# Optimization experiments

Hardware: AMD Instinct MI355X
Metric: run time of the kernel (lower is better)

The kernel has to match this reference:

```python
import jax, jax.numpy as jnp
import numpy as np

D_MODEL = 4096
N_EXPERTS = 64
TOKENS = 16384


def setup_inputs() -> dict:
    key = jax.random.key(0)
    kx, kw = jax.random.split(key)
    x = jax.random.normal(kx, (TOKENS, D_MODEL), dtype=jnp.float32)
    # nn.Linear(d_model, n_experts, bias=False) weight: [E, d_model]
    wg = jax.random.normal(kw, (N_EXPERTS, D_MODEL), dtype=jnp.float32) * (1.0 / np.sqrt(D_MODEL))
    return {"x": x, "wg": wg, "k": 2}


def reference(x, wg, k):
    S = x.shape[0]
    E = wg.shape[0]
    logits = jnp.einsum('sd,ed->se', x, wg)        # [S, E]
    probs = jax.nn.softmax(logits, axis=-1)        # [S, E]
    topk_vals, topk_idx = jax.lax.top_k(probs, k)  # [S, k] each
    importance = probs.mean(axis=0)                # [E]
    hard1 = topk_idx[:, 0]                         # [S]
    load = jax.ops.segment_sum(jnp.ones((S,), probs.dtype), hard1,
                               num_segments=E) / S  # [E]
    aux_load = E * (importance * load).sum()
    return (topk_idx, topk_vals, aux_load)
```

## Files before the change

kernel.cpp:

```cpp
#include <hip/hip_runtime.h>
#include <cmath>

#define TOKENS 16384
#define DM     4096
#define NEXP   64
#define S_W    64.0f
#define S_LO   2048.0f

typedef _Float16 half8 __attribute__((ext_vector_type(8)));
typedef float    f32x4 __attribute__((ext_vector_type(4)));


__global__ __launch_bounds__(64)
void prep_kernel(const float* __restrict__ wg, _Float16* __restrict__ whB,
                 _Float16* __restrict__ wlB, float* __restrict__ gsum)
{
    const int kb = blockIdx.x >> 2;
    const int et = blockIdx.x & 3;
    const int l  = threadIdx.x;
    const int e  = et * 16 + (l & 15);
    const int k0 = kb * 32 + 8 * (l >> 4);

    const float* wp = wg + (size_t)e * DM + k0;
    float v[8];
    *(float4*)(v)     = *(const float4*)(wp);
    *(float4*)(v + 4) = *(const float4*)(wp + 4);

    half8 hh, ll;
    #pragma unroll
    for (int j = 0; j < 8; ++j) {
        const float ws = v[j] * S_W;
        const _Float16 h = (_Float16)ws;
        hh[j] = h;
        ll[j] = (_Float16)((ws - (float)h) * S_LO);
    }
    const int idx = blockIdx.x * 64 + l;
    ((half8*)whB)[idx] = hh;
    ((half8*)wlB)[idx] = ll;

    if (blockIdx.x == 0) { gsum[l] = 0.f; gsum[64 + l] = 0.f; }
}

__global__ __launch_bounds__(256)
void moe_kernel(const float* __restrict__ x, const _Float16* __restrict__ whB,
                const _Float16* __restrict__ wlB, float* __restrict__ out,
                float* __restrict__ gsum)
{
    const int lane  = threadIdx.x & 63;
    const int wave  = threadIdx.x >> 6;
    const int tgrp  = wave & 1;
    const int khalf = wave >> 1;
    const int sub   = lane & 15;
    const int q     = lane >> 4;
    const int t0    = blockIdx.x * 32 + tgrp * 16;

    f32x4 ahh[4] = {};
    f32x4 amd[4] = {};

    const float* xp = x + (size_t)(t0 + sub) * DM + 8 * q;
    const half8* whv = (const half8*)whB;
    const half8* wlv = (const half8*)wlB;

    const int kb0 = khalf * 64, kbe = kb0 + 64;
    float4 a0 = *(const float4*)(xp + kb0 * 32);
    float4 a1 = *(const float4*)(xp + kb0 * 32 + 4);

    for (int kb = kb0; kb < kbe; ++kb) {
        const int kn = (kb + 1 < kbe) ? kb + 1 : kb;
        float4 n0 = *(const float4*)(xp + kn * 32);
        float4 n1 = *(const float4*)(xp + kn * 32 + 4);

        half8 bh[4], bl[4];
        const int bbase = kb * 256 + lane;
        #pragma unroll
        for (int et = 0; et < 4; ++et) {
            bh[et] = whv[bbase + et * 64];
            bl[et] = wlv[bbase + et * 64];
        }

        float v[8];
        *(float4*)(v)     = a0;
        *(float4*)(v + 4) = a1;
        half8 xh, xl;
        #pragma unroll
        for (int j = 0; j < 8; ++j) {
            const _Float16 h = (_Float16)v[j];
            xh[j] = h;
            xl[j] = (_Float16)((v[j] - (float)h) * S_LO);
        }

        #pragma unroll
        for (int et = 0; et < 4; ++et) {
            ahh[et] = __builtin_amdgcn_mfma_f32_16x16x32_f16(xh, bh[et], ahh[et], 0, 0, 0);
            amd[et] = __builtin_amdgcn_mfma_f32_16x16x32_f16(xh, bl[et], amd[et], 0, 0, 0);
            amd[et] = __builtin_amdgcn_mfma_f32_16x16x32_f16(xl, bh[et], amd[et], 0, 0, 0);
        }
        a0 = n0; a1 = n1;
    }

    float lg[4][4];
    #pragma unroll
    for (int et = 0; et < 4; ++et)
        #pragma unroll
        for (int r = 0; r < 4; ++r)
            lg[et][r] = (ahh[et][r] + amd[et][r] * (1.0f / S_LO)) * (1.0f / S_W);

    __shared__ float lmerge[2][16][64];
    __shared__ float bimp[2][64], bcnt[2][64];

    if (khalf == 1) {
        #pragma unroll
        for (int et = 0; et < 4; ++et)
            #pragma unroll
            for (int r = 0; r < 4; ++r)
                lmerge[tgrp][4 * q + r][sub + 16 * et] = lg[et][r];
    }
    __syncthreads();

    if (khalf == 0) {
        float imp[4] = {0, 0, 0, 0}, cnt[4] = {0, 0, 0, 0};
        #pragma unroll
        for (int et = 0; et < 4; ++et)
            #pragma unroll
            for (int r = 0; r < 4; ++r)
                lg[et][r] += lmerge[tgrp][4 * q + r][sub + 16 * et];

        for (int r = 0; r < 4; ++r) {
            const int tok = t0 + 4 * q + r;
            float m = fmaxf(fmaxf(lg[0][r], lg[1][r]), fmaxf(lg[2][r], lg[3][r]));
            #pragma unroll
            for (int off = 1; off < 16; off <<= 1) m = fmaxf(m, __shfl_xor(m, off));
            float p[4]; float s = 0.f;
            #pragma unroll
            for (int et = 0; et < 4; ++et) { p[et] = expf(lg[et][r] - m); s += p[et]; }
            #pragma unroll
            for (int off = 1; off < 16; off <<= 1) s += __shfl_xor(s, off);
            #pragma unroll
            for (int et = 0; et < 4; ++et) p[et] = p[et] / s;

            float v1, v2; int i1, i2;
            if (p[1] > p[0]) { v1 = p[1]; i1 = sub + 16; v2 = p[0]; i2 = sub; }
            else             { v1 = p[0]; i1 = sub;      v2 = p[1]; i2 = sub + 16; }
            #pragma unroll
            for (int et = 2; et < 4; ++et) {
                const float vv = p[et]; const int id = sub + 16 * et;
                if (vv > v1)      { v2 = v1; i2 = i1; v1 = vv; i1 = id; }
                else if (vv > v2) { v2 = vv; i2 = id; }
            }
            #pragma unroll
            for (int off = 1; off < 16; off <<= 1) {
                const float w1 = __shfl_xor(v1, off), w2 = __shfl_xor(v2, off);
                const int   j1 = __shfl_xor(i1, off), j2 = __shfl_xor(i2, off);
                if (w1 > v1 || (w1 == v1 && j1 < i1)) {
                    if (v1 > w2 || (v1 == w2 && i1 < j2)) { v2 = v1; i2 = i1; }
                    else                                   { v2 = w2; i2 = j2; }
                    v1 = w1; i1 = j1;
                } else {
                    if (w1 > v2 || (w1 == v2 && j1 < i2)) { v2 = w1; i2 = j1; }
                }
            }

            if (sub == 0) {
                out[2 * tok]                  = (float)i1;
                out[2 * tok + 1]              = (float)i2;
                out[2 * TOKENS + 2 * tok]     = v1;
                out[2 * TOKENS + 2 * tok + 1] = v2;
            }
            #pragma unroll
            for (int et = 0; et < 4; ++et) {
                imp[et] += p[et];
                if (i1 == sub + 16 * et) cnt[et] += 1.0f;
            }
        }
        #pragma unroll
        for (int et = 0; et < 4; ++et) {
            imp[et] += __shfl_xor(imp[et], 16); imp[et] += __shfl_xor(imp[et], 32);
            cnt[et] += __shfl_xor(cnt[et], 16); cnt[et] += __shfl_xor(cnt[et], 32);
        }
        if (q == 0) {
            #pragma unroll
            for (int et = 0; et < 4; ++et) {
                bimp[tgrp][sub + 16 * et] = imp[et];
                bcnt[tgrp][sub + 16 * et] = cnt[et];
            }
        }
    }
    __syncthreads();

    if (wave == 0) {
        atomicAdd(gsum + lane,      bimp[0][lane] + bimp[1][lane]);
        atomicAdd(gsum + 64 + lane, bcnt[0][lane] + bcnt[1][lane]);
    }
}

__global__ __launch_bounds__(64)
void aux_kernel(const float* __restrict__ gsum, float* __restrict__ out)
{
    const int l = threadIdx.x;
    float prod = gsum[l] * gsum[64 + l];
    #pragma unroll
    for (int off = 32; off; off >>= 1) prod += __shfl_xor(prod, off);
    if (l == 0)
        out[4 * TOKENS] = (float)NEXP * prod / ((float)TOKENS * (float)TOKENS);
}

extern "C" void kernel_launch(void* const* d_in, const int* in_sizes, int n_in,
                              void* d_out, int out_size, void* d_ws, size_t ws_size,
                              hipStream_t stream) {
    const float* x  = (const float*)d_in[0];
    const float* wg = (const float*)d_in[1];
    float* out = (float*)d_out;

    _Float16* whB = (_Float16*)d_ws;
    _Float16* wlB = whB + 262144;
    float*    gsum = (float*)(wlB + 262144);

    prep_kernel<<<512, 64, 0, stream>>>(wg, whB, wlB, gsum);
    moe_kernel<<<512, 256, 0, stream>>>(x, whB, wlB, out, gsum);
    aux_kernel<<<1, 64, 0, stream>>>(gsum, out);
}
```

Baseline: 405.5 us.

## Deepen x prefetch, double-buffer weights, fuse aux reduction into main kernel

```diff
diff --git a/kernel.cpp b/kernel.cpp
--- a/kernel.cpp
+++ b/kernel.cpp
@@ -7,8 +7,9 @@
 #define S_W    64.0f
 #define S_LO   2048.0f
 
-typedef _Float16 half8 __attribute__((ext_vector_type(8)));
-typedef float    f32x4 __attribute__((ext_vector_type(4)));
+typedef _Float16 half8  __attribute__((ext_vector_type(8)));
+typedef __fp16   h2rtz  __attribute__((ext_vector_type(2)));
+typedef float    f32x4  __attribute__((ext_vector_type(4)));
 
 
 __global__ __launch_bounds__(64)
@@ -23,8 +24,8 @@
 
     const float* wp = wg + (size_t)e * DM + k0;
     float v[8];
-    *(float4*)(v)     = *(const float4*)(wp);
-    *(float4*)(v + 4) = *(const float4*)(wp + 4);
+    *(f32x4*)(v)     = *(const f32x4*)(wp);
+    *(f32x4*)(v + 4) = *(const f32x4*)(wp + 4);
 
     half8 hh, ll;
     #pragma unroll
@@ -38,10 +39,45 @@
     ((half8*)whB)[idx] = hh;
     ((half8*)wlB)[idx] = ll;
 
-    if (blockIdx.x == 0) { gsum[l] = 0.f; gsum[64 + l] = 0.f; }
-}
-
-__global__ __launch_bounds__(256)
+    if (blockIdx.x == 0) {
+        gsum[l] = 0.f; gsum[64 + l] = 0.f;
+        if (l == 0) *(unsigned*)(gsum + 128) = 0u;
+    }
+}
+
+__device__ __forceinline__ void split8(const f32x4& a0, const f32x4& a1,
+                                       half8& xh, half8& xl)
+{
+    float v[8];
+    *(f32x4*)(v)     = a0;
+    *(f32x4*)(v + 4) = a1;
+    h2rtz h01 = __builtin_amdgcn_cvt_pkrtz(v[0], v[1]);
+    h2rtz h23 = __builtin_amdgcn_cvt_pkrtz(v[2], v[3]);
+    h2rtz h45 = __builtin_amdgcn_cvt_pkrtz(v[4], v[5]);
+    h2rtz h67 = __builtin_amdgcn_cvt_pkrtz(v[6], v[7]);
+    xh[0] = (_Float16)h01[0]; xh[1] = (_Float16)h01[1];
+    xh[2] = (_Float16)h23[0]; xh[3] = (_Float16)h23[1];
+    xh[4] = (_Float16)h45[0]; xh[5] = (_Float16)h45[1];
+    xh[6] = (_Float16)h67[0]; xh[7] = (_Float16)h67[1];
+    const float r0 = (v[0] - (float)h01[0]) * S_LO;
+    const float r1 = (v[1] - (float)h01[1]) * S_LO;
+    const float r2 = (v[2] - (float)h23[0]) * S_LO;
+    const float r3 = (v[3] - (float)h23[1]) * S_LO;
+    const float r4 = (v[4] - (float)h45[0]) * S_LO;
+    const float r5 = (v[5] - (float)h45[1]) * S_LO;
+    const float r6 = (v[6] - (float)h67[0]) * S_LO;
+    const float r7 = (v[7] - (float)h67[1]) * S_LO;
+    h2rtz l01 = __builtin_amdgcn_cvt_pkrtz(r0, r1);
+    h2rtz l23 = __builtin_amdgcn_cvt_pkrtz(r2, r3);
+    h2rtz l45 = __builtin_amdgcn_cvt_pkrtz(r4, r5);
+    h2rtz l67 = __builtin_amdgcn_cvt_pkrtz(r6, r7);
+    xl[0] = (_Float16)l01[0]; xl[1] = (_Float16)l01[1];
+    xl[2] = (_Float16)l23[0]; xl[3] = (_Float16)l23[1];
+    xl[4] = (_Float16)l45[0]; xl[5] = (_Float16)l45[1];
+    xl[6] = (_Float16)l67[0]; xl[7] = (_Float16)l67[1];
+}
+
+__global__ __launch_bounds__(256, 2)
 void moe_kernel(const float* __restrict__ x, const _Float16* __restrict__ whB,
                 const _Float16* __restrict__ wlB, float* __restrict__ out,
                 float* __restrict__ gsum)
@@ -62,40 +98,48 @@
     const half8* wlv = (const half8*)wlB;
 
     const int kb0 = khalf * 64, kbe = kb0 + 64;
-    float4 a0 = *(const float4*)(xp + kb0 * 32);
-    float4 a1 = *(const float4*)(xp + kb0 * 32 + 4);
-
-    for (int kb = kb0; kb < kbe; ++kb) {
-        const int kn = (kb + 1 < kbe) ? kb + 1 : kb;
-        float4 n0 = *(const float4*)(xp + kn * 32);
-        float4 n1 = *(const float4*)(xp + kn * 32 + 4);
-
-        half8 bh[4], bl[4];
-        const int bbase = kb * 256 + lane;
-        #pragma unroll
-        for (int et = 0; et < 4; ++et) {
-            bh[et] = whv[bbase + et * 64];
-            bl[et] = wlv[bbase + et * 64];
-        }
-
-        float v[8];
-        *(float4*)(v)     = a0;
-        *(float4*)(v + 4) = a1;
-        half8 xh, xl;
-        #pragma unroll
-        for (int j = 0; j < 8; ++j) {
-            const _Float16 h = (_Float16)v[j];
-            xh[j] = h;
-            xl[j] = (_Float16)((v[j] - (float)h) * S_LO);
-        }
-
-        #pragma unroll
-        for (int et = 0; et < 4; ++et) {
-            ahh[et] = __builtin_amdgcn_mfma_f32_16x16x32_f16(xh, bh[et], ahh[et], 0, 0, 0);
-            amd[et] = __builtin_amdgcn_mfma_f32_16x16x32_f16(xh, bl[et], amd[et], 0, 0, 0);
-            amd[et] = __builtin_amdgcn_mfma_f32_16x16x32_f16(xl, bh[et], amd[et], 0, 0, 0);
-        }
-        a0 = n0; a1 = n1;
+
+    f32x4 ra0[4], ra1[4];
+    #pragma unroll
+    for (int d = 0; d < 3; ++d) {
+        ra0[d] = __builtin_nontemporal_load((const f32x4*)(xp + (kb0 + d) * 32));
+        ra1[d] = __builtin_nontemporal_load((const f32x4*)(xp + (kb0 + d) * 32 + 4));
+    }
+
+    half8 bh[2][4], bl[2][4];
+    #pragma unroll
+    for (int et = 0; et < 4; ++et) {
+        bh[0][et] = whv[kb0 * 256 + lane + et * 64];
+        bl[0][et] = wlv[kb0 * 256 + lane + et * 64];
+    }
+
+    for (int kb = kb0; kb < kbe; kb += 4) {
+        #pragma unroll
+        for (int u = 0; u < 4; ++u) {
+            const int k = kb + u;
+
+            const int kpf = (k + 3 < kbe) ? k + 3 : kbe - 1;
+            ra0[(u + 3) & 3] = __builtin_nontemporal_load((const f32x4*)(xp + kpf * 32));
+            ra1[(u + 3) & 3] = __builtin_nontemporal_load((const f32x4*)(xp + kpf * 32 + 4));
+
+            const int knb = (k + 1 < kbe) ? k + 1 : kbe - 1;
+            const int cur = u & 1, nxt = cur ^ 1;
+            #pragma unroll
+            for (int et = 0; et < 4; ++et) {
+                bh[nxt][et] = whv[knb * 256 + lane + et * 64];
+                bl[nxt][et] = wlv[knb * 256 + lane + et * 64];
+            }
+
+            half8 xh, xl;
+            split8(ra0[u], ra1[u], xh, xl);
+
+            #pragma unroll
+            for (int et = 0; et < 4; ++et) {
+                ahh[et] = __builtin_amdgcn_mfma_f32_16x16x32_f16(xh, bh[cur][et], ahh[et], 0, 0, 0);
+                amd[et] = __builtin_amdgcn_mfma_f32_16x16x32_f16(xh, bl[cur][et], amd[et], 0, 0, 0);
+                amd[et] = __builtin_amdgcn_mfma_f32_16x16x32_f16(xl, bh[cur][et], amd[et], 0, 0, 0);
+            }
+        }
     }
 
     float lg[4][4];
@@ -190,18 +234,24 @@
     if (wave == 0) {
         atomicAdd(gsum + lane,      bimp[0][lane] + bimp[1][lane]);
         atomicAdd(gsum + 64 + lane, bcnt[0][lane] + bcnt[1][lane]);
-    }
-}
-
-__global__ __launch_bounds__(64)
-void aux_kernel(const float* __restrict__ gsum, float* __restrict__ out)
-{
-    const int l = threadIdx.x;
-    float prod = gsum[l] * gsum[64 + l];
-    #pragma unroll
-    for (int off = 32; off; off >>= 1) prod += __shfl_xor(prod, off);
-    if (l == 0)
-        out[4 * TOKENS] = (float)NEXP * prod / ((float)TOKENS * (float)TOKENS);
+        __threadfence();
+        int last = 0;
+        if (lane == 0) {
+            unsigned old = atomicAdd((unsigned*)(gsum + 128), 1u);
+            last = (old == 511u);
+        }
+        last = __shfl(last, 0);
+        if (last) {
+            __threadfence();
+            const float a = atomicAdd(gsum + lane, 0.f);
+            const float b = atomicAdd(gsum + 64 + lane, 0.f);
+            float prod = a * b;
+            #pragma unroll
+            for (int off = 32; off; off >>= 1) prod += __shfl_xor(prod, off);
+            if (lane == 0)
+                out[4 * TOKENS] = (float)NEXP * prod / ((float)TOKENS * (float)TOKENS);
+        }
+    }
 }
 
 extern "C" void kernel_launch(void* const* d_in, const int* in_sizes, int n_in,
@@ -217,5 +267,4 @@
 
     prep_kernel<<<512, 64, 0, stream>>>(wg, whB, wlB, gsum);
     moe_kernel<<<512, 256, 0, stream>>>(x, whB, wlB, out, gsum);
-    aux_kernel<<<1, 64, 0, stream>>>(gsum, out);
-}
+}
```

New measurement: 404.5 us. About the same (-0.2%).
